# Performance work log

Measured on AMD Instinct MI355X. Metric: run time of the kernel, lower is better.

## Reference

```python
import jax, jax.numpy as jnp
import numpy as np

EMB_DIM = 256
Q_DIM = 512
V_DIM = 512

def setup_inputs() -> dict:
    key = jax.random.key(0)
    ks = jax.random.split(key, 7)
    B, S = 8, 2048
    x = jax.random.normal(ks[0], (B, S, EMB_DIM), dtype=jnp.float32)
    s = 1.0 / np.sqrt(EMB_DIM)
    Wq = jax.random.normal(ks[1], (EMB_DIM, Q_DIM), dtype=jnp.float32) * s
    bq = jax.random.normal(ks[2], (Q_DIM,), dtype=jnp.float32) * 0.01
    Wk = jax.random.normal(ks[3], (EMB_DIM, Q_DIM), dtype=jnp.float32) * s
    bk = jax.random.normal(ks[4], (Q_DIM,), dtype=jnp.float32) * 0.01
    Wv = jax.random.normal(ks[5], (EMB_DIM, V_DIM), dtype=jnp.float32) * s
    bv = jax.random.normal(ks[6], (V_DIM,), dtype=jnp.float32) * 0.01
    return {"x": x, "Wq": Wq, "bq": bq, "Wk": Wk, "bk": bk, "Wv": Wv, "bv": bv}

def reference(x, Wq, bq, Wk, bk, Wv, bv):
    # q/k/v projections (torch Linear == x @ W + b with W stored [in, out] here)
    q = jax.nn.sigmoid(jnp.einsum('bse,eq->bsq', x, Wq) + bq)   # [B,S,Q]
    k = jnp.einsum('bse,eq->bsq', x, Wk) + bk                   # [B,S,Q]
    v = jnp.einsum('bse,ev->bsv', x, Wv) + bv                   # [B,S,V]
    scale = 1.0 / jnp.sqrt(jnp.float32(EMB_DIM))
    qk = jnp.einsum('bsq,btq->bst', q, k) * scale               # [B,S,S]
    qk = jax.nn.elu(qk)
    attn = jax.nn.softmax(qk, axis=-1)
    return jnp.einsum('bst,btv->bsv', attn, v)                  # [B,S,V]
```

## Files before the change

kernel.cpp:

```cpp
#include <hip/hip_runtime.h>
#include <hip/hip_bf16.h>
#include <math.h>

typedef unsigned short u16;
using short8 = __attribute__((ext_vector_type(8))) short;
using f32x4  = __attribute__((ext_vector_type(4))) float;

#define BK 32


__device__ __forceinline__ u16 f2bf(float f) {
  union { float f; unsigned u; } v; v.f = f;
  unsigned r = v.u + 0x7FFFu + ((v.u >> 16) & 1u);
  return (u16)(r >> 16);
}

__device__ __forceinline__ float fexp(float x) { return __expf(x); }

__device__ __forceinline__ void gld16(const void* g, void* l) {
  __builtin_amdgcn_global_load_lds(
      (const __attribute__((address_space(1))) void*)g,
      (__attribute__((address_space(3))) void*)l,
      16, 0, 0);
}


__device__ __forceinline__ void gemm_core4(const u16* __restrict__ Ag,
                                           const u16* __restrict__ Bg,
                                           int K, int lda, int ldb,
                                           u16* As, u16* Bs,
                                           f32x4 acc[4][4], int w, int l) {
  const int wm = (w & 1) << 6, wn = (w >> 1) << 6;
  const int ln = l & 15, lq = l >> 4;
  const int sr0 = w * 16 + (l >> 2);
  const int sr1 = 64 + sr0;
  const int sk = (l & 3) * 8;

#pragma unroll
  for (int mt = 0; mt < 4; mt++)
#pragma unroll
    for (int nt = 0; nt < 4; nt++) acc[mt][nt] = (f32x4)0.0f;

  for (int k0 = 0; k0 < K; k0 += BK) {
    __syncthreads();
    gld16(Ag + (size_t)sr0 * lda + k0 + sk, As + sr0 * BK + sk);
    gld16(Ag + (size_t)sr1 * lda + k0 + sk, As + sr1 * BK + sk);
    gld16(Bg + (size_t)sr0 * ldb + k0 + sk, Bs + sr0 * BK + sk);
    gld16(Bg + (size_t)sr1 * ldb + k0 + sk, Bs + sr1 * BK + sk);
    __syncthreads();
    short8 af[4], bf[4];
#pragma unroll
    for (int mt = 0; mt < 4; mt++)
      af[mt] = *(const short8*)(As + (wm + mt * 16 + ln) * BK + lq * 8);
#pragma unroll
    for (int nt = 0; nt < 4; nt++)
      bf[nt] = *(const short8*)(Bs + (wn + nt * 16 + ln) * BK + lq * 8);
#pragma unroll
    for (int mt = 0; mt < 4; mt++)
#pragma unroll
      for (int nt = 0; nt < 4; nt++)
        acc[mt][nt] = __builtin_amdgcn_mfma_f32_16x16x32_bf16(
            af[mt], bf[nt], acc[mt][nt], 0, 0, 0);
  }
}


__global__ __launch_bounds__(256) void k_conv(
    const float* __restrict__ x, u16* __restrict__ xb,
    const float* __restrict__ Wq, const float* __restrict__ Wk,
    const float* __restrict__ Wv, const float* __restrict__ bq,
    const float* __restrict__ bk, const float* __restrict__ bv,
    u16* __restrict__ Wt, float* __restrict__ bcat) {
  const int bid = blockIdx.x;
  if (bid < 4096) {
    int i = bid * 256 + threadIdx.x;
    float4 v = ((const float4*)x)[i];
    ushort4 o;
    o.x = f2bf(v.x); o.y = f2bf(v.y); o.z = f2bf(v.z); o.w = f2bf(v.w);
    ((ushort4*)xb)[i] = o;
  } else {
    int i = (bid - 4096) * 256 + threadIdx.x;
    int nn = i >> 8, e = i & 255;
    int sel = nn >> 9, c = nn & 511;
    const float* W = (sel == 0) ? Wq : (sel == 1) ? Wk : Wv;
    Wt[i] = f2bf(W[e * 512 + c]);
    if (e == 0) {
      const float* bb = (sel == 0) ? bq : (sel == 1) ? bk : bv;
      bcat[nn] = bb[c];
    }
  }
}


__global__ __launch_bounds__(256) void k_proj(
    const u16* __restrict__ xb, const u16* __restrict__ Wt,
    const float* __restrict__ bcat, u16* __restrict__ qb,
    u16* __restrict__ kb, u16* __restrict__ vtb) {
  __shared__ __align__(16) u16 smem[8704];
  u16* As = smem;
  u16* Bs = smem + 4096;
  const int bm = blockIdx.y * 128, bn = blockIdx.x * 128;
  const int tid = threadIdx.x, w = tid >> 6, l = tid & 63;
  f32x4 acc[4][4];
  gemm_core4(xb + (size_t)bm * 256, Wt + (size_t)bn * 256, 256, 256, 256,
             As, Bs, acc, w, l);

  const int wm = (w & 1) << 6, wn = (w >> 1) << 6;
  const int ln = l & 15, lq = l >> 4;
  const int sel = blockIdx.x >> 2;
  const int cb = (blockIdx.x & 3) * 128;

  if (sel < 2) {
    u16* dst = sel ? kb : qb;
#pragma unroll
    for (int mt = 0; mt < 4; mt++)
#pragma unroll
      for (int r = 0; r < 4; r++) {
        int row = bm + wm + mt * 16 + lq * 4 + r;
#pragma unroll
        for (int nt = 0; nt < 4; nt++) {
          int col = wn + nt * 16 + ln;
          float v = acc[mt][nt][r] + bcat[bn + col];
          float ov = (sel == 0) ? __builtin_amdgcn_rcpf(1.0f + fexp(-v)) : v;
          dst[(size_t)row * 512 + cb + col] = f2bf(ov);
        }
      }
  } else {
    const int b = bm >> 11, t0 = bm & 2047;
#pragma unroll
    for (int h = 0; h < 2; h++) {
      __syncthreads();
      if ((w & 1) == h) {
#pragma unroll
        for (int mt = 0; mt < 4; mt++)
#pragma unroll
          for (int nt = 0; nt < 4; nt++) {
            int c = wn + nt * 16 + ln;
            float bias = bcat[bn + c];
#pragma unroll
            for (int r = 0; r < 4; r++) {
              int lr = mt * 16 + lq * 4 + r;
              smem[c * 68 + lr] = f2bf(acc[mt][nt][r] + bias);
            }
          }
      }
      __syncthreads();
      int c2 = tid >> 1, half = tid & 1;
      size_t dbase = ((size_t)b * 512 + cb + c2) * 2048 + t0 + h * 64 + half * 32;
#pragma unroll
      for (int j = 0; j < 4; j++) {
        ushort4 a0 = *(const ushort4*)&smem[c2 * 68 + half * 32 + j * 8];
        ushort4 a1 = *(const ushort4*)&smem[c2 * 68 + half * 32 + j * 8 + 4];
        *(ushort4*)&vtb[dbase + j * 8] = a0;
        *(ushort4*)&vtb[dbase + j * 8 + 4] = a1;
      }
    }
  }
}


__global__ __launch_bounds__(256, 4) void k_qk(const u16* __restrict__ qb,
                                               const u16* __restrict__ kb,
                                               u16* __restrict__ P,
                                               float* __restrict__ lsum) {
  __shared__ __align__(16) u16 As[128 * BK];
  __shared__ __align__(16) u16 Bs[128 * BK];
  const int b = blockIdx.z;
  const int bm = blockIdx.y * 128, bn = blockIdx.x * 128;
  const size_t ob = (size_t)b * 2048 * 512;
  const int tid = threadIdx.x, w = tid >> 6, l = tid & 63;
  f32x4 acc[4][4];
  gemm_core4(qb + ob + (size_t)bm * 512, kb + ob + (size_t)bn * 512,
             512, 512, 512, As, Bs, acc, w, l);

  const int wm = (w & 1) << 6, wn = (w >> 1) << 6;
  const int ln = l & 15, lq = l >> 4;
  const float scale = 0.0625f;
#pragma unroll
  for (int mt = 0; mt < 4; mt++)
#pragma unroll
    for (int r = 0; r < 4; r++) {
      int row = bm + wm + mt * 16 + lq * 4 + r;
      float s = 0.0f;
#pragma unroll
      for (int nt = 0; nt < 4; nt++) {
        int col = bn + wn + nt * 16 + ln;
        float v = acc[mt][nt][r] * scale;
        float e = (v > 0.0f) ? v : (fexp(v) - 1.0f);
        float p = fexp(e);
        P[((size_t)b * 2048 + row) * 2048 + col] = f2bf(p);
        s += p;
      }
#pragma unroll
      for (int o = 1; o < 16; o <<= 1) s += __shfl_xor(s, o);
      if (ln == 0) atomicAdd(&lsum[b * 2048 + row], s);
    }
}


__global__ __launch_bounds__(256) void k_pv(const u16* __restrict__ P,
                                            const u16* __restrict__ vtb,
                                            const float* __restrict__ lsum,
                                            float* __restrict__ out) {
  __shared__ __align__(16) u16 As[128 * BK];
  __shared__ __align__(16) u16 Bs[128 * BK];
  const int b = blockIdx.z;
  const int bm = blockIdx.y * 128, bn = blockIdx.x * 128;
  const int tid = threadIdx.x, w = tid >> 6, l = tid & 63;
  f32x4 acc[4][4];
  gemm_core4(P  + (size_t)b * 2048 * 2048 + (size_t)bm * 2048,
             vtb + (size_t)b * 512 * 2048 + (size_t)bn * 2048,
             2048, 2048, 2048, As, Bs, acc, w, l);

  const int wm = (w & 1) << 6, wn = (w >> 1) << 6;
  const int ln = l & 15, lq = l >> 4;
#pragma unroll
  for (int mt = 0; mt < 4; mt++)
#pragma unroll
    for (int r = 0; r < 4; r++) {
      int row = bm + wm + mt * 16 + lq * 4 + r;
      float inv = 1.0f / lsum[b * 2048 + row];
#pragma unroll
      for (int nt = 0; nt < 4; nt++) {
        int col = bn + wn + nt * 16 + ln;
        out[((size_t)b * 2048 + row) * 512 + col] = acc[mt][nt][r] * inv;
      }
    }
}


extern "C" void kernel_launch(void* const* d_in, const int* in_sizes, int n_in,
                              void* d_out, int out_size, void* d_ws, size_t ws_size,
                              hipStream_t stream) {
  const float* x  = (const float*)d_in[0];
  const float* Wq = (const float*)d_in[1];
  const float* bq = (const float*)d_in[2];
  const float* Wk = (const float*)d_in[3];
  const float* bk = (const float*)d_in[4];
  const float* Wv = (const float*)d_in[5];
  const float* bv = (const float*)d_in[6];
  float* out = (float*)d_out;
  char* ws = (char*)d_ws;

  u16*  qb   = (u16*)(ws + 0);
  u16*  kb   = (u16*)(ws + 16777216);
  u16*  vtb  = (u16*)(ws + 33554432);
  float* lsum = (float*)(ws + 50331648);
  u16*  P    = (u16*)(ws + 50397184);
  u16*  xb   = (u16*)(ws + 50397184);
  u16*  Wt   = (u16*)(ws + 58785792);
  float* bcat = (float*)(ws + 59572224);

  k_conv<<<5632, 256, 0, stream>>>(x, xb, Wq, Wk, Wv, bq, bk, bv, Wt, bcat);
  k_proj<<<dim3(12, 128, 1), 256, 0, stream>>>(xb, Wt, bcat, qb, kb, vtb);
  hipMemsetAsync(lsum, 0, 16384 * sizeof(float), stream);
  k_qk<<<dim3(16, 16, 8), 256, 0, stream>>>(qb, kb, P, lsum);
  k_pv<<<dim3(4, 16, 8), 256, 0, stream>>>(P, vtb, lsum, out);
}
```

Baseline: 228.5 us.

## Switch GEMM core to 32x32x16 MFMA and interleave batches across blocks

Replaces the 16x16x32 bf16 MFMA tiling with 32x32x16 MFMA (2x2 tiles of 32x32 per wave, two k-halves per BK=32 step), and remaps the epilogue row and column indices for all three GEMM kernels to match. It also flattens the qk and pv grids so that the batch index is the fastest-varying block index, spreading batches across CUs and XCDs, and adds a launch bound of 4 blocks per CU to k_pv. The larger MFMA shape gives more work per instruction and per LDS fragment read, which should reduce issue overhead. The cost is a more involved epilogue index mapping and possibly more LDS bank conflicts.

```diff
diff --git a/kernel.cpp b/kernel.cpp
--- a/kernel.cpp
+++ b/kernel.cpp
@@ -5,6 +5,7 @@
 typedef unsigned short u16;
 using short8 = __attribute__((ext_vector_type(8))) short;
 using f32x4  = __attribute__((ext_vector_type(4))) float;
+using f32x16 = __attribute__((ext_vector_type(16))) float;
 
 #define BK 32
 
@@ -25,21 +26,21 @@
 }
 
 
-__device__ __forceinline__ void gemm_core4(const u16* __restrict__ Ag,
-                                           const u16* __restrict__ Bg,
-                                           int K, int lda, int ldb,
-                                           u16* As, u16* Bs,
-                                           f32x4 acc[4][4], int w, int l) {
-  const int wm = (w & 1) << 6, wn = (w >> 1) << 6;
-  const int ln = l & 15, lq = l >> 4;
+__device__ __forceinline__ void gemm_core32(const u16* __restrict__ Ag,
+                                            const u16* __restrict__ Bg,
+                                            int K, int lda, int ldb,
+                                            u16* As, u16* Bs,
+                                            f32x16 acc[2][2], int w, int l) {
+  const int wm = (w & 1) << 6, wn = (w >> 1) << 6;
+  const int ln = l & 31, l5 = l >> 5;
   const int sr0 = w * 16 + (l >> 2);
   const int sr1 = 64 + sr0;
   const int sk = (l & 3) * 8;
 
 #pragma unroll
-  for (int mt = 0; mt < 4; mt++)
-#pragma unroll
-    for (int nt = 0; nt < 4; nt++) acc[mt][nt] = (f32x4)0.0f;
+  for (int mt = 0; mt < 2; mt++)
+#pragma unroll
+    for (int nt = 0; nt < 2; nt++) acc[mt][nt] = (f32x16)0.0f;
 
   for (int k0 = 0; k0 < K; k0 += BK) {
     __syncthreads();
@@ -48,19 +49,25 @@
     gld16(Bg + (size_t)sr0 * ldb + k0 + sk, Bs + sr0 * BK + sk);
     gld16(Bg + (size_t)sr1 * ldb + k0 + sk, Bs + sr1 * BK + sk);
     __syncthreads();
-    short8 af[4], bf[4];
-#pragma unroll
-    for (int mt = 0; mt < 4; mt++)
-      af[mt] = *(const short8*)(As + (wm + mt * 16 + ln) * BK + lq * 8);
-#pragma unroll
-    for (int nt = 0; nt < 4; nt++)
-      bf[nt] = *(const short8*)(Bs + (wn + nt * 16 + ln) * BK + lq * 8);
-#pragma unroll
-    for (int mt = 0; mt < 4; mt++)
-#pragma unroll
-      for (int nt = 0; nt < 4; nt++)
-        acc[mt][nt] = __builtin_amdgcn_mfma_f32_16x16x32_bf16(
-            af[mt], bf[nt], acc[mt][nt], 0, 0, 0);
+    short8 af[2][2], bf[2][2];
+#pragma unroll
+    for (int mt = 0; mt < 2; mt++)
+#pragma unroll
+      for (int kh = 0; kh < 2; kh++)
+        af[mt][kh] = *(const short8*)(As + (wm + mt * 32 + ln) * BK + kh * 16 + l5 * 8);
+#pragma unroll
+    for (int nt = 0; nt < 2; nt++)
+#pragma unroll
+      for (int kh = 0; kh < 2; kh++)
+        bf[nt][kh] = *(const short8*)(Bs + (wn + nt * 32 + ln) * BK + kh * 16 + l5 * 8);
+#pragma unroll
+    for (int mt = 0; mt < 2; mt++)
+#pragma unroll
+      for (int nt = 0; nt < 2; nt++)
+#pragma unroll
+        for (int kh = 0; kh < 2; kh++)
+          acc[mt][nt] = __builtin_amdgcn_mfma_f32_32x32x16_bf16(
+              af[mt][kh], bf[nt][kh], acc[mt][nt], 0, 0, 0);
   }
 }
 
@@ -101,25 +108,25 @@
   u16* Bs = smem + 4096;
   const int bm = blockIdx.y * 128, bn = blockIdx.x * 128;
   const int tid = threadIdx.x, w = tid >> 6, l = tid & 63;
-  f32x4 acc[4][4];
-  gemm_core4(xb + (size_t)bm * 256, Wt + (size_t)bn * 256, 256, 256, 256,
-             As, Bs, acc, w, l);
-
-  const int wm = (w & 1) << 6, wn = (w >> 1) << 6;
-  const int ln = l & 15, lq = l >> 4;
+  f32x16 acc[2][2];
+  gemm_core32(xb + (size_t)bm * 256, Wt + (size_t)bn * 256, 256, 256, 256,
+              As, Bs, acc, w, l);
+
+  const int wm = (w & 1) << 6, wn = (w >> 1) << 6;
+  const int ln = l & 31, l5 = l >> 5;
   const int sel = blockIdx.x >> 2;
   const int cb = (blockIdx.x & 3) * 128;
 
   if (sel < 2) {
     u16* dst = sel ? kb : qb;
 #pragma unroll
-    for (int mt = 0; mt < 4; mt++)
-#pragma unroll
-      for (int r = 0; r < 4; r++) {
-        int row = bm + wm + mt * 16 + lq * 4 + r;
-#pragma unroll
-        for (int nt = 0; nt < 4; nt++) {
-          int col = wn + nt * 16 + ln;
+    for (int mt = 0; mt < 2; mt++)
+#pragma unroll
+      for (int r = 0; r < 16; r++) {
+        int row = bm + wm + mt * 32 + (r & 3) + 8 * (r >> 2) + 4 * l5;
+#pragma unroll
+        for (int nt = 0; nt < 2; nt++) {
+          int col = wn + nt * 32 + ln;
           float v = acc[mt][nt][r] + bcat[bn + col];
           float ov = (sel == 0) ? __builtin_amdgcn_rcpf(1.0f + fexp(-v)) : v;
           dst[(size_t)row * 512 + cb + col] = f2bf(ov);
@@ -132,17 +139,17 @@
       __syncthreads();
       if ((w & 1) == h) {
 #pragma unroll
-        for (int mt = 0; mt < 4; mt++)
-#pragma unroll
-          for (int nt = 0; nt < 4; nt++) {
-            int c = wn + nt * 16 + ln;
-            float bias = bcat[bn + c];
-#pragma unroll
-            for (int r = 0; r < 4; r++) {
-              int lr = mt * 16 + lq * 4 + r;
+        for (int nt = 0; nt < 2; nt++) {
+          int c = wn + nt * 32 + ln;
+          float bias = bcat[bn + c];
+#pragma unroll
+          for (int mt = 0; mt < 2; mt++)
+#pragma unroll
+            for (int r = 0; r < 16; r++) {
+              int lr = mt * 32 + (r & 3) + 8 * (r >> 2) + 4 * l5;
               smem[c * 68 + lr] = f2bf(acc[mt][nt][r] + bias);
             }
-          }
+        }
       }
       __syncthreads();
       int c2 = tid >> 1, half = tid & 1;
@@ -165,26 +172,27 @@
                                                float* __restrict__ lsum) {
   __shared__ __align__(16) u16 As[128 * BK];
   __shared__ __align__(16) u16 Bs[128 * BK];
-  const int b = blockIdx.z;
-  const int bm = blockIdx.y * 128, bn = blockIdx.x * 128;
+  const int bid = blockIdx.x;
+  const int b = bid & 7, t = bid >> 3;
+  const int bm = (t >> 4) * 128, bn = (t & 15) * 128;
   const size_t ob = (size_t)b * 2048 * 512;
   const int tid = threadIdx.x, w = tid >> 6, l = tid & 63;
-  f32x4 acc[4][4];
-  gemm_core4(qb + ob + (size_t)bm * 512, kb + ob + (size_t)bn * 512,
-             512, 512, 512, As, Bs, acc, w, l);
-
-  const int wm = (w & 1) << 6, wn = (w >> 1) << 6;
-  const int ln = l & 15, lq = l >> 4;
+  f32x16 acc[2][2];
+  gemm_core32(qb + ob + (size_t)bm * 512, kb + ob + (size_t)bn * 512,
+              512, 512, 512, As, Bs, acc, w, l);
+
+  const int wm = (w & 1) << 6, wn = (w >> 1) << 6;
+  const int ln = l & 31, l5 = l >> 5;
   const float scale = 0.0625f;
 #pragma unroll
-  for (int mt = 0; mt < 4; mt++)
-#pragma unroll
-    for (int r = 0; r < 4; r++) {
-      int row = bm + wm + mt * 16 + lq * 4 + r;
+  for (int mt = 0; mt < 2; mt++)
+#pragma unroll
+    for (int r = 0; r < 16; r++) {
+      int row = bm + wm + mt * 32 + (r & 3) + 8 * (r >> 2) + 4 * l5;
       float s = 0.0f;
 #pragma unroll
-      for (int nt = 0; nt < 4; nt++) {
-        int col = bn + wn + nt * 16 + ln;
+      for (int nt = 0; nt < 2; nt++) {
+        int col = bn + wn + nt * 32 + ln;
         float v = acc[mt][nt][r] * scale;
         float e = (v > 0.0f) ? v : (fexp(v) - 1.0f);
         float p = fexp(e);
@@ -192,37 +200,38 @@
         s += p;
       }
 #pragma unroll
-      for (int o = 1; o < 16; o <<= 1) s += __shfl_xor(s, o);
+      for (int o = 1; o < 32; o <<= 1) s += __shfl_xor(s, o);
       if (ln == 0) atomicAdd(&lsum[b * 2048 + row], s);
     }
 }
 
 
-__global__ __launch_bounds__(256) void k_pv(const u16* __restrict__ P,
-                                            const u16* __restrict__ vtb,
-                                            const float* __restrict__ lsum,
-                                            float* __restrict__ out) {
+__global__ __launch_bounds__(256, 4) void k_pv(const u16* __restrict__ P,
+                                               const u16* __restrict__ vtb,
+                                               const float* __restrict__ lsum,
+                                               float* __restrict__ out) {
   __shared__ __align__(16) u16 As[128 * BK];
   __shared__ __align__(16) u16 Bs[128 * BK];
-  const int b = blockIdx.z;
-  const int bm = blockIdx.y * 128, bn = blockIdx.x * 128;
+  const int bid = blockIdx.x;
+  const int b = bid & 7, t = bid >> 3;
+  const int bm = (t >> 2) * 128, bn = (t & 3) * 128;
   const int tid = threadIdx.x, w = tid >> 6, l = tid & 63;
-  f32x4 acc[4][4];
-  gemm_core4(P  + (size_t)b * 2048 * 2048 + (size_t)bm * 2048,
-             vtb + (size_t)b * 512 * 2048 + (size_t)bn * 2048,
-             2048, 2048, 2048, As, Bs, acc, w, l);
-
-  const int wm = (w & 1) << 6, wn = (w >> 1) << 6;
-  const int ln = l & 15, lq = l >> 4;
-#pragma unroll
-  for (int mt = 0; mt < 4; mt++)
-#pragma unroll
-    for (int r = 0; r < 4; r++) {
-      int row = bm + wm + mt * 16 + lq * 4 + r;
+  f32x16 acc[2][2];
+  gemm_core32(P  + (size_t)b * 2048 * 2048 + (size_t)bm * 2048,
+              vtb + (size_t)b * 512 * 2048 + (size_t)bn * 2048,
+              2048, 2048, 2048, As, Bs, acc, w, l);
+
+  const int wm = (w & 1) << 6, wn = (w >> 1) << 6;
+  const int ln = l & 31, l5 = l >> 5;
+#pragma unroll
+  for (int mt = 0; mt < 2; mt++)
+#pragma unroll
+    for (int r = 0; r < 16; r++) {
+      int row = bm + wm + mt * 32 + (r & 3) + 8 * (r >> 2) + 4 * l5;
       float inv = 1.0f / lsum[b * 2048 + row];
 #pragma unroll
-      for (int nt = 0; nt < 4; nt++) {
-        int col = bn + wn + nt * 16 + ln;
+      for (int nt = 0; nt < 2; nt++) {
+        int col = bn + wn + nt * 32 + ln;
         out[((size_t)b * 2048 + row) * 512 + col] = acc[mt][nt][r] * inv;
       }
     }
@@ -254,6 +263,6 @@
   k_conv<<<5632, 256, 0, stream>>>(x, xb, Wq, Wk, Wv, bq, bk, bv, Wt, bcat);
   k_proj<<<dim3(12, 128, 1), 256, 0, stream>>>(xb, Wt, bcat, qb, kb, vtb);
   hipMemsetAsync(lsum, 0, 16384 * sizeof(float), stream);
-  k_qk<<<dim3(16, 16, 8), 256, 0, stream>>>(qb, kb, P, lsum);
-  k_pv<<<dim3(4, 16, 8), 256, 0, stream>>>(P, vtb, lsum, out);
-}
+  k_qk<<<2048, 256, 0, stream>>>(qb, kb, P, lsum);
+  k_pv<<<512, 256, 0, stream>>>(P, vtb, lsum, out);
+}
```

New measurement: 246.0 us. 7.7% more time.

## Swizzle LDS tiles in GEMM core and remap grids to interleave batches

Applied to the files above, without the earlier changes.

The shared GEMM core now permutes which 16-byte k-chunk each lane fetches from global memory (XOR on row bits), and the MFMA fragment reads use the matching XOR offset. This is meant to cut LDS bank conflicts on the short8 reads from the 32-wide rows. The QK and PV kernels move from 3D grids to 1D grids with the batch index in the low bits, which spreads concurrent blocks across batches and may change L2/MALL locality. k_pv also gains an occupancy hint of 4 blocks per CU, which may force register limits.

```diff
diff --git a/kernel.cpp b/kernel.cpp
--- a/kernel.cpp
+++ b/kernel.cpp
@@ -34,7 +34,9 @@
   const int ln = l & 15, lq = l >> 4;
   const int sr0 = w * 16 + (l >> 2);
   const int sr1 = 64 + sr0;
-  const int sk = (l & 3) * 8;
+  const int skp = (l & 3) * 8;
+  const int skg = ((l & 3) ^ ((l >> 3) & 3)) * 8;
+  const int kro = (lq ^ ((ln >> 1) & 3)) * 8;
 
 #pragma unroll
   for (int mt = 0; mt < 4; mt++)
@@ -43,18 +45,18 @@
 
   for (int k0 = 0; k0 < K; k0 += BK) {
     __syncthreads();
-    gld16(Ag + (size_t)sr0 * lda + k0 + sk, As + sr0 * BK + sk);
-    gld16(Ag + (size_t)sr1 * lda + k0 + sk, As + sr1 * BK + sk);
-    gld16(Bg + (size_t)sr0 * ldb + k0 + sk, Bs + sr0 * BK + sk);
-    gld16(Bg + (size_t)sr1 * ldb + k0 + sk, Bs + sr1 * BK + sk);
+    gld16(Ag + (size_t)sr0 * lda + k0 + skg, As + sr0 * BK + skp);
+    gld16(Ag + (size_t)sr1 * lda + k0 + skg, As + sr1 * BK + skp);
+    gld16(Bg + (size_t)sr0 * ldb + k0 + skg, Bs + sr0 * BK + skp);
+    gld16(Bg + (size_t)sr1 * ldb + k0 + skg, Bs + sr1 * BK + skp);
     __syncthreads();
     short8 af[4], bf[4];
 #pragma unroll
     for (int mt = 0; mt < 4; mt++)
-      af[mt] = *(const short8*)(As + (wm + mt * 16 + ln) * BK + lq * 8);
+      af[mt] = *(const short8*)(As + (wm + mt * 16 + ln) * BK + kro);
 #pragma unroll
     for (int nt = 0; nt < 4; nt++)
-      bf[nt] = *(const short8*)(Bs + (wn + nt * 16 + ln) * BK + lq * 8);
+      bf[nt] = *(const short8*)(Bs + (wn + nt * 16 + ln) * BK + kro);
 #pragma unroll
     for (int mt = 0; mt < 4; mt++)
 #pragma unroll
@@ -165,8 +167,9 @@
                                                float* __restrict__ lsum) {
   __shared__ __align__(16) u16 As[128 * BK];
   __shared__ __align__(16) u16 Bs[128 * BK];
-  const int b = blockIdx.z;
-  const int bm = blockIdx.y * 128, bn = blockIdx.x * 128;
+  const int bid = blockIdx.x;
+  const int b = bid & 7, t = bid >> 3;
+  const int bm = (t >> 4) * 128, bn = (t & 15) * 128;
   const size_t ob = (size_t)b * 2048 * 512;
   const int tid = threadIdx.x, w = tid >> 6, l = tid & 63;
   f32x4 acc[4][4];
@@ -198,14 +201,15 @@
 }
 
 
-__global__ __launch_bounds__(256) void k_pv(const u16* __restrict__ P,
-                                            const u16* __restrict__ vtb,
-                                            const float* __restrict__ lsum,
-                                            float* __restrict__ out) {
+__global__ __launch_bounds__(256, 4) void k_pv(const u16* __restrict__ P,
+                                               const u16* __restrict__ vtb,
+                                               const float* __restrict__ lsum,
+                                               float* __restrict__ out) {
   __shared__ __align__(16) u16 As[128 * BK];
   __shared__ __align__(16) u16 Bs[128 * BK];
-  const int b = blockIdx.z;
-  const int bm = blockIdx.y * 128, bn = blockIdx.x * 128;
+  const int bid = blockIdx.x;
+  const int b = bid & 7, t = bid >> 3;
+  const int bm = (t >> 2) * 128, bn = (t & 3) * 128;
   const int tid = threadIdx.x, w = tid >> 6, l = tid & 63;
   f32x4 acc[4][4];
   gemm_core4(P  + (size_t)b * 2048 * 2048 + (size_t)bm * 2048,
@@ -254,6 +258,6 @@
   k_conv<<<5632, 256, 0, stream>>>(x, xb, Wq, Wk, Wv, bq, bk, bv, Wt, bcat);
   k_proj<<<dim3(12, 128, 1), 256, 0, stream>>>(xb, Wt, bcat, qb, kb, vtb);
   hipMemsetAsync(lsum, 0, 16384 * sizeof(float), stream);
-  k_qk<<<dim3(16, 16, 8), 256, 0, stream>>>(qb, kb, P, lsum);
-  k_pv<<<dim3(4, 16, 8), 256, 0, stream>>>(P, vtb, lsum, out);
-}
+  k_qk<<<2048, 256, 0, stream>>>(qb, kb, P, lsum);
+  k_pv<<<512, 256, 0, stream>>>(P, vtb, lsum, out);
+}
```

After: 216.7 us. -5.2%, faster.
